# Kernel optimization log

Hardware: AMD Instinct MI355X
Metric: run time of the kernel (lower is better)

The kernel has to match this reference:

```python
import jax, jax.numpy as jnp
import numpy as np

# Dims: B samples, D=2048 backbone feature dim (resnet50 fc.in_features),
B, D, G, R, K, C = 16384, 2048, 8, 6, 3, 16


def setup_inputs() -> dict:
    key = jax.random.key(0)
    k0, k1, k2, k3 = jax.random.split(key, 4)
    feats = jax.random.normal(k0, (B, D), dtype=jnp.float32)          # backbone output (dropout=eval identity)
    roi_ids = jax.random.randint(k1, (B,), 0, G)                       # per-sample routing id (roi_names)
    W_reg = jax.random.normal(k2, (G, R, D), dtype=jnp.float32) * 0.02  # reg_heads[roi].weight
    b_reg = jnp.zeros((G, R), dtype=jnp.float32)                       # reg_heads[roi].bias
    W_cls = jax.random.normal(k3, (G, K, C, D), dtype=jnp.float32) * 0.02  # cls_heads[roi][k].weight
    b_cls = jnp.zeros((G, K, C), dtype=jnp.float32)                    # cls_heads[roi][k].bias
    return {"feats": feats, "roi_ids": roi_ids, "W_reg": W_reg, "b_reg": b_reg,
            "W_cls": W_cls, "b_cls": b_cls}


def reference(feats, roi_ids, W_reg, b_reg, W_cls, b_cls):
    # Original loop applies, per sample i, the Linear heads of roi_names[i].
    # Vectorized: compute all-ROI head outputs densely, then gather the routed one.
    # (Same math per sample; dropout is identity in eval mode.)
    reg_all = jnp.einsum('bd,grd->bgr', feats, W_reg) + b_reg[None]        # [B, G, R]
    cls_all = jnp.einsum('bd,gkcd->bgkc', feats, W_cls) + b_cls[None]      # [B, G, K, C]
    reg = jnp.take_along_axis(reg_all, roi_ids[:, None, None], axis=1)[:, 0]            # [B, R]
    cls = jnp.take_along_axis(cls_all, roi_ids[:, None, None, None], axis=1)[:, 0]      # [B, K, C]
    return reg, cls
```

## Files before the change

kernel.cpp:

```cpp
#include <hip/hip_runtime.h>
#include <hip/hip_bf16.h>

#define NB   16384
#define NG   8
#define ND   2048
#define NR   6
#define NKC  48
#define NOUT 54
#define NT16 (NB / 16 + NG)
#define LROW 136
#define BM   32
#define KC   128
#define NCH  (ND / KC)
#define MAXT (NB / BM + NG)

typedef __attribute__((ext_vector_type(8))) short short8_t;
typedef __attribute__((ext_vector_type(4))) float f32x4;

__device__ __forceinline__ unsigned short f2bf(float x) {
    union { float f; unsigned u; } v; v.f = x;
    unsigned r = v.u + 0x7FFFu + ((v.u >> 16) & 1u);
    return (unsigned short)(r >> 16);
}

__device__ __forceinline__ short8_t cvt8(float4 a, float4 b) {
    short8_t s;
    s[0] = (short)f2bf(a.x); s[1] = (short)f2bf(a.y);
    s[2] = (short)f2bf(a.z); s[3] = (short)f2bf(a.w);
    s[4] = (short)f2bf(b.x); s[5] = (short)f2bf(b.y);
    s[6] = (short)f2bf(b.z); s[7] = (short)f2bf(b.w);
    return s;
}

__device__ __forceinline__ void gl_lds16(const void* g, void* s) {
    __builtin_amdgcn_global_load_lds(
        (const __attribute__((address_space(1))) void*)g,
        (__attribute__((address_space(3))) void*)s,
        16, 0, 0);
}

#define WAITV(N) do { asm volatile("s_waitcnt vmcnt(" #N ")" ::: "memory"); \
                      __builtin_amdgcn_sched_barrier(0); } while (0)
#define BAR() do { __builtin_amdgcn_s_barrier(); \
                   __builtin_amdgcn_sched_barrier(0); } while (0)

__global__ void hist_kernel(const int* __restrict__ roi, int* __restrict__ counts) {
    int i = blockIdx.x * 256 + threadIdx.x;
    int g = roi[i];
    int lane = threadIdx.x & 63;
    #pragma unroll
    for (int gg = 0; gg < NG; ++gg) {
        unsigned long long m = __ballot(g == gg);
        if (m && lane == (int)(__ffsll((unsigned long long)m) - 1))
            atomicAdd(&counts[gg], (int)__popcll(m));
    }
}

__global__ void scatter_kernel(const int* __restrict__ roi, const int* __restrict__ counts,
                               int* __restrict__ ranks, int* __restrict__ perm) {
    int off[NG];
    int acc = 0;
    #pragma unroll
    for (int gg = 0; gg < NG; ++gg) { off[gg] = acc; acc += counts[gg]; }
    int i = blockIdx.x * 256 + threadIdx.x;
    int g = roi[i];
    int lane = threadIdx.x & 63;
    #pragma unroll
    for (int gg = 0; gg < NG; ++gg) {
        unsigned long long m = __ballot(g == gg);
        if (!m) continue;
        int leader = (int)(__ffsll((unsigned long long)m) - 1);
        int base = 0;
        if (lane == leader) base = atomicAdd(&ranks[gg], (int)__popcll(m));
        base = __shfl(base, leader);
        if (g == gg) {
            int rank = (int)__popcll(m & ((1ull << lane) - 1ull));
            perm[off[gg] + base + rank] = i;
        }
    }
}

__global__ void prep_kernel(const int* __restrict__ roi, int* __restrict__ cnt,
                            int* __restrict__ perm,
                            const float* __restrict__ Wreg, const float* __restrict__ Wcls,
                            short* __restrict__ Wbf) {
    if (blockIdx.x < 64) {
        int i = blockIdx.x * 256 + threadIdx.x;
        int g = roi[i];
        int lane = threadIdx.x & 63;
        #pragma unroll
        for (int gg = 0; gg < NG; ++gg) {
            unsigned long long m = __ballot(g == gg);
            if (!m) continue;
            int leader = (int)(__ffsll((unsigned long long)m) - 1);
            int base = 0;
            if (lane == leader) base = atomicAdd(&cnt[gg], (int)__popcll(m));
            base = __shfl(base, leader);
            if (g == gg) {
                int rank = (int)__popcll(m & ((1ull << lane) - 1ull));
                perm[gg * NB + base + rank] = i;
            }
        }
    } else {
        int u = (blockIdx.x - 64) * 256 + threadIdx.x;
        int l = u & 63;
        int q = (u >> 6) & 7;
        int c = (u >> 9) & 31;
        int g = u >> 14;
        int n = q >> 1, ks = q & 1;
        int row = n * 16 + (l & 15);
        int k   = c * 64 + ks * 32 + (l >> 4) * 8;
        short8_t v = {0, 0, 0, 0, 0, 0, 0, 0};
        if (row < NOUT) {
            const float* s = (row < NR) ? Wreg + (size_t)(g * NR + row) * ND + k
                                        : Wcls + (size_t)(g * NKC + row - NR) * ND + k;
            float4 a = *(const float4*)s;
            float4 b = *(const float4*)(s + 4);
            v = cvt8(a, b);
        }
        *(short8_t*)(Wbf + (size_t)u * 8) = v;
    }
}

__launch_bounds__(256, 4)
__global__ void gemm16_kernel(const float* __restrict__ feats,
                              const short* __restrict__ Wbf,
                              const float* __restrict__ breg, const float* __restrict__ bcls,
                              const int* __restrict__ cnt, const int* __restrict__ perm,
                              float* __restrict__ out) {
    __shared__ __align__(16) char lds[3][12288];
    __shared__ int sRow[16];

    int tid = threadIdx.x, w = tid >> 6, l = tid & 63, lr = l & 15, lq = l >> 4;

    int ts[NG + 1]; ts[0] = 0;
    #pragma unroll
    for (int gg = 0; gg < NG; ++gg) ts[gg + 1] = ts[gg] + ((cnt[gg] + 15) >> 4);
    int b = blockIdx.x;
    if (b >= ts[NG]) return;
    int g = 0;
    #pragma unroll
    for (int gg = 0; gg < NG; ++gg) if (b >= ts[gg + 1]) g = gg + 1;
    int cg = cnt[g];
    int rbase = (b - ts[g]) * 16;
    int nv = cg - rbase; if (nv > 16) nv = 16;

    if (tid < 16) {
        int r = rbase + tid;
        if (r >= cg) r = cg - 1;
        sRow[tid] = perm[g * NB + r];
    }
    __syncthreads();

    int srow = 4 * w + lq;
    const char* aSrc = (const char*)(feats + (size_t)sRow[srow] * ND)
                     + (((l & 15) ^ (srow & 7)) << 4);
    const char* bSrc = (const char*)Wbf + (size_t)g * 262144 + (2 * w) * 1024 + l * 16;

    const int key = lr & 7;
    const int ra00 = lr * 256 + (((0 * 8 + lq * 2 + 0) ^ key) << 4);
    const int ra01 = lr * 256 + (((0 * 8 + lq * 2 + 1) ^ key) << 4);
    const int ra10 = lr * 256 + (((1 * 8 + lq * 2 + 0) ^ key) << 4);
    const int ra11 = lr * 256 + (((1 * 8 + lq * 2 + 1) ^ key) << 4);
    const int rb0  = 4096 + (2 * w + 0) * 1024 + l * 16;
    const int rb1  = 4096 + (2 * w + 1) * 1024 + l * 16;

#define STAGE(cc, sl) do {                                                     \
        gl_lds16(aSrc + (size_t)(cc) * 256, &lds[sl][w * 1024]);               \
        const char* b_ = bSrc + (size_t)(cc) * 8192;                           \
        gl_lds16(b_,        &lds[sl][4096 + 2 * w * 1024]);                    \
        gl_lds16(b_ + 1024, &lds[sl][4096 + 2 * w * 1024 + 1024]);             \
    } while (0)

    f32x4 acc = {0, 0, 0, 0};

    STAGE(0, 0); STAGE(1, 1);
    int csl = 0;
    #pragma unroll
    for (int c = 0; c < 32; ++c) {
        if (c + 2 < 32) STAGE(c + 2, (c + 2) % 3);
        if (c < 30)       WAITV(6);
        else if (c == 30) WAITV(3);
        else              WAITV(0);
        BAR();
        {
            const char* s = &lds[csl][0];
            float4 a0 = *(const float4*)(s + ra00);
            float4 a1 = *(const float4*)(s + ra01);
            short8_t af0 = cvt8(a0, a1);
            short8_t b0  = *(const short8_t*)(s + rb0);
            acc = __builtin_amdgcn_mfma_f32_16x16x32_bf16(af0, b0, acc, 0, 0, 0);
            float4 a2 = *(const float4*)(s + ra10);
            float4 a3 = *(const float4*)(s + ra11);
            short8_t af1 = cvt8(a2, a3);
            short8_t b1  = *(const short8_t*)(s + rb1);
            acc = __builtin_amdgcn_mfma_f32_16x16x32_bf16(af1, b1, acc, 0, 0, 0);
        }
        BAR();
        csl = (csl == 2) ? 0 : csl + 1;
    }
#undef STAGE

    const int B6 = NB * NR;
    int col = w * 16 + lr;
    if (col < NOUT) {
        #pragma unroll
        for (int j = 0; j < 4; ++j) {
            int row = lq * 4 + j;
            if (row < nv) {
                int smp = sRow[row];
                if (col < NR) out[smp * NR + col] = acc[j] + breg[g * NR + col];
                else          out[B6 + smp * NKC + (col - NR)] = acc[j] + bcls[g * NKC + (col - NR)];
            }
        }
    }
}

__launch_bounds__(256, 3)
__global__ void gemm_kernel(const float* __restrict__ feats,
                            const float* __restrict__ Wreg, const float* __restrict__ breg,
                            const float* __restrict__ Wcls, const float* __restrict__ bcls,
                            const int* __restrict__ counts, const int* __restrict__ perm,
                            float* __restrict__ out, int stride) {
    __shared__ __align__(16) short Bsh[2][64][LROW];
    __shared__ int sRow[BM];

    int ts[NG + 1]; ts[0] = 0;
    int off[NG]; int acc = 0;
    #pragma unroll
    for (int gg = 0; gg < NG; ++gg) {
        int c = counts[gg];
        off[gg] = stride ? gg * stride : acc;
        acc += c;
        ts[gg + 1] = ts[gg] + (c + BM - 1) / BM;
    }
    int b = blockIdx.x;
    if (b >= ts[NG]) return;
    int g = 0;
    #pragma unroll
    for (int gg = 0; gg < NG; ++gg) if (b >= ts[gg + 1]) g = gg + 1;
    int gcnt  = counts[g];
    int goff  = off[g];
    int rbase = (b - ts[g]) * BM;
    int nvalid = gcnt - rbase; if (nvalid > BM) nvalid = BM;

    int tid = threadIdx.x;
    if (tid < BM) {
        int r = rbase + tid;
        if (r >= gcnt) r = gcnt - 1;
        sRow[tid] = perm[goff + r];
    }
    __syncthreads();

    int rB = tid >> 2;
    int cq = tid & 3;
    const float* wsrc = nullptr;
    if (rB < NR)        wsrc = Wreg + ((size_t)g * NR + rB) * ND + cq * 32;
    else if (rB < NOUT) wsrc = Wcls + ((size_t)g * NKC + (rB - NR)) * ND + cq * 32;

    int w = tid >> 6, l = tid & 63, lr = l & 15, lq = l >> 4;
    int mt = w & 1, nh = w >> 1;
    const float* aptr = feats + (size_t)sRow[mt * 16 + lr] * ND + lq * 8;
    const short* brp = (const short*)&Bsh[0][0][0] + (nh * 32 + lr) * LROW + lq * 8;

    f32x4 acc0 = {0, 0, 0, 0}, acc1 = {0, 0, 0, 0};
    float4 rb[8];

    if (wsrc) {
        #pragma unroll
        for (int i = 0; i < 8; ++i) rb[i] = *(const float4*)(wsrc + 4 * i);
    } else {
        #pragma unroll
        for (int i = 0; i < 8; ++i) rb[i] = make_float4(0.f, 0.f, 0.f, 0.f);
    }
    {
        short* bw = &Bsh[0][rB][cq * 32];
        #pragma unroll
        for (int j = 0; j < 4; ++j) *(short8_t*)(bw + 8 * j) = cvt8(rb[2 * j], rb[2 * j + 1]);
    }
    __syncthreads();

    #pragma unroll
    for (int c = 0; c < NCH; ++c) {
        const int cur = c & 1, nxt = cur ^ 1;
        if (c + 1 < NCH && wsrc) {
            const float* s = wsrc + (c + 1) * KC;
            #pragma unroll
            for (int i = 0; i < 8; ++i) rb[i] = *(const float4*)(s + 4 * i);
        }
        const short* bp = brp + cur * (64 * LROW);
        const float* ap = aptr + c * KC;
        #pragma unroll
        for (int ks = 0; ks < 4; ++ks) {
            float4 a0 = *(const float4*)(ap + ks * 32);
            float4 a1 = *(const float4*)(ap + ks * 32 + 4);
            short8_t af = cvt8(a0, a1);
            short8_t b0 = *(const short8_t*)(bp + ks * 32);
            short8_t b1 = *(const short8_t*)(bp + 16 * LROW + ks * 32);
            acc0 = __builtin_amdgcn_mfma_f32_16x16x32_bf16(af, b0, acc0, 0, 0, 0);
            acc1 = __builtin_amdgcn_mfma_f32_16x16x32_bf16(af, b1, acc1, 0, 0, 0);
        }
        if (c + 1 < NCH && wsrc) {
            short* bw = &Bsh[nxt][rB][cq * 32];
            #pragma unroll
            for (int j = 0; j < 4; ++j) *(short8_t*)(bw + 8 * j) = cvt8(rb[2 * j], rb[2 * j + 1]);
        } else if (c + 1 < NCH) {
            short8_t z = {0,0,0,0,0,0,0,0};
            short* bw = &Bsh[nxt][rB][cq * 32];
            #pragma unroll
            for (int j = 0; j < 4; ++j) *(short8_t*)(bw + 8 * j) = z;
        }
        __syncthreads();
    }

    const int B6 = NB * NR;
    #pragma unroll
    for (int n = 0; n < 2; ++n) {
        f32x4 v = n ? acc1 : acc0;
        int col = nh * 32 + n * 16 + lr;
        if (col < NOUT) {
            #pragma unroll
            for (int j = 0; j < 4; ++j) {
                int row = mt * 16 + lq * 4 + j;
                if (row < nvalid) {
                    int smp = sRow[row];
                    if (col < NR) out[smp * NR + col] = v[j] + breg[g * NR + col];
                    else          out[B6 + smp * NKC + (col - NR)] = v[j] + bcls[g * NKC + (col - NR)];
                }
            }
        }
    }
}

__global__ void fallback_kernel(const float* __restrict__ feats, const int* __restrict__ roi,
                                const float* __restrict__ Wreg, const float* __restrict__ breg,
                                const float* __restrict__ Wcls, const float* __restrict__ bcls,
                                float* __restrict__ out) {
    int i = blockIdx.x;
    int lane = threadIdx.x;
    int g = roi[i];
    const float* frow = feats + (size_t)i * ND;
    float f[32];
    #pragma unroll
    for (int q = 0; q < 32; ++q) f[q] = frow[lane + 64 * q];
    for (int o = 0; o < NOUT; ++o) {
        const float* wrow = (o < NR) ? Wreg + ((size_t)g * NR + o) * ND
                                     : Wcls + ((size_t)g * NKC + (o - NR)) * ND;
        float p = 0.f;
        #pragma unroll
        for (int q = 0; q < 32; ++q) p += f[q] * wrow[lane + 64 * q];
        #pragma unroll
        for (int s = 32; s; s >>= 1) p += __shfl_xor(p, s);
        if (lane == 0) {
            if (o < NR) out[i * NR + o] = p + breg[g * NR + o];
            else        out[NB * NR + i * NKC + (o - NR)] = p + bcls[g * NKC + (o - NR)];
        }
    }
}

extern "C" void kernel_launch(void* const* d_in, const int* in_sizes, int n_in,
                              void* d_out, int out_size, void* d_ws, size_t ws_size,
                              hipStream_t stream) {
    const float* feats = (const float*)d_in[0];
    const int*   roi   = (const int*)d_in[1];
    const float* Wreg  = (const float*)d_in[2];
    const float* breg  = (const float*)d_in[3];
    const float* Wcls  = (const float*)d_in[4];
    const float* bcls  = (const float*)d_in[5];
    float* out = (float*)d_out;

    const size_t wbfBytes = (size_t)NG * 131072 * 2;
    const size_t need_t1 = wbfBytes + 256 + (size_t)NG * NB * 4;
    const size_t need_t3 = 256 + (size_t)NB * 4;

    if (ws_size >= need_t1) {
        short* Wbf = (short*)d_ws;
        int* cnt   = (int*)((char*)d_ws + wbfBytes);
        int* perm  = cnt + 64;
        hipMemsetAsync(cnt, 0, 64, stream);
        prep_kernel<<<576, 256, 0, stream>>>(roi, cnt, perm, Wreg, Wcls, Wbf);
        gemm16_kernel<<<NT16, 256, 0, stream>>>(feats, Wbf, breg, bcls, cnt, perm, out);
    } else if (ws_size >= need_t3) {
        int* counts = (int*)d_ws;
        int* ranks  = counts + 8;
        int* perm   = counts + 64;
        hipMemsetAsync(counts, 0, 16 * sizeof(int), stream);
        hist_kernel<<<NB / 256, 256, 0, stream>>>(roi, counts);
        scatter_kernel<<<NB / 256, 256, 0, stream>>>(roi, counts, ranks, perm);
        gemm_kernel<<<MAXT, 256, 0, stream>>>(feats, Wreg, breg, Wcls, bcls, counts, perm, out, 0);
    } else {
        fallback_kernel<<<NB, 64, 0, stream>>>(feats, roi, Wreg, breg, Wcls, bcls, out);
    }
}
```

Baseline: 73.81 us.

## Replace 16-row GEMM with 64-row split-K tiles and six-stage LDS pipeline

```diff
diff --git a/kernel.cpp b/kernel.cpp
--- a/kernel.cpp
+++ b/kernel.cpp
@@ -7,7 +7,6 @@
 #define NR   6
 #define NKC  48
 #define NOUT 54
-#define NT16 (NB / 16 + NG)
 #define LROW 136
 #define BM   32
 #define KC   128
@@ -122,95 +121,107 @@
     }
 }
 
-__launch_bounds__(256, 4)
-__global__ void gemm16_kernel(const float* __restrict__ feats,
-                              const short* __restrict__ Wbf,
-                              const float* __restrict__ breg, const float* __restrict__ bcls,
-                              const int* __restrict__ cnt, const int* __restrict__ perm,
-                              float* __restrict__ out) {
-    __shared__ __align__(16) char lds[3][12288];
-    __shared__ int sRow[16];
+__launch_bounds__(512, 1)
+__global__ void gemm_d6_kernel(const float* __restrict__ feats,
+                               const short* __restrict__ Wbf,
+                               const float* __restrict__ breg, const float* __restrict__ bcls,
+                               const int* __restrict__ cnt, const int* __restrict__ perm,
+                               float* __restrict__ out) {
+    __shared__ __align__(16) char lds[6][24576];
+    __shared__ int sRow[64];
 
     int tid = threadIdx.x, w = tid >> 6, l = tid & 63, lr = l & 15, lq = l >> 4;
+    int rw = w >> 1, ch = w & 1;
 
     int ts[NG + 1]; ts[0] = 0;
     #pragma unroll
-    for (int gg = 0; gg < NG; ++gg) ts[gg + 1] = ts[gg] + ((cnt[gg] + 15) >> 4);
-    int b = blockIdx.x;
-    if (b >= ts[NG]) return;
+    for (int gg = 0; gg < NG; ++gg) ts[gg + 1] = ts[gg] + ((cnt[gg] + 63) >> 6);
+    int item = blockIdx.x;
+    if (item >= 2 * ts[NG]) return;
+    int t = item >> 1, kh = item & 1;
     int g = 0;
     #pragma unroll
-    for (int gg = 0; gg < NG; ++gg) if (b >= ts[gg + 1]) g = gg + 1;
+    for (int gg = 0; gg < NG; ++gg) if (t >= ts[gg + 1]) g = gg + 1;
     int cg = cnt[g];
-    int rbase = (b - ts[g]) * 16;
-    int nv = cg - rbase; if (nv > 16) nv = 16;
-
-    if (tid < 16) {
+    int rbase = (t - ts[g]) * 64;
+    int nv = cg - rbase; if (nv > 64) nv = 64;
+
+    if (tid < 64) {
         int r = rbase + tid;
         if (r >= cg) r = cg - 1;
         sRow[tid] = perm[g * NB + r];
     }
     __syncthreads();
 
-    int srow = 4 * w + lq;
-    const char* aSrc = (const char*)(feats + (size_t)sRow[srow] * ND)
-                     + (((l & 15) ^ (srow & 7)) << 4);
-    const char* bSrc = (const char*)Wbf + (size_t)g * 262144 + (2 * w) * 1024 + l * 16;
-
+    int r0 = 8 * w + (l >> 4), r1 = r0 + 4;
+    const char* a0c = (const char*)(feats + (size_t)sRow[r0] * ND) + kh * 4096
+                    + (((l & 15) ^ (r0 & 7)) << 4);
+    const char* a1c = (const char*)(feats + (size_t)sRow[r1] * ND) + kh * 4096
+                    + (((l & 15) ^ (r1 & 7)) << 4);
+    const char* bSrc = (const char*)Wbf + ((size_t)(g * 32 + kh * 16) * 8 + w) * 1024 + l * 16;
+
+#define STAGE(cc, sl) do {                                                     \
+        gl_lds16(a0c + (size_t)(cc) * 256,  &lds[sl][w * 2048]);               \
+        gl_lds16(a1c + (size_t)(cc) * 256,  &lds[sl][w * 2048 + 1024]);        \
+        gl_lds16(bSrc + (size_t)(cc) * 8192, &lds[sl][16384 + w * 1024]);      \
+    } while (0)
+
+    f32x4 acc0 = {0, 0, 0, 0}, acc1 = {0, 0, 0, 0};
+
+    STAGE(0, 0); STAGE(1, 1); STAGE(2, 2); STAGE(3, 3);
+
+    const int abase = (rw * 16 + lr) * 256;
     const int key = lr & 7;
-    const int ra00 = lr * 256 + (((0 * 8 + lq * 2 + 0) ^ key) << 4);
-    const int ra01 = lr * 256 + (((0 * 8 + lq * 2 + 1) ^ key) << 4);
-    const int ra10 = lr * 256 + (((1 * 8 + lq * 2 + 0) ^ key) << 4);
-    const int ra11 = lr * 256 + (((1 * 8 + lq * 2 + 1) ^ key) << 4);
-    const int rb0  = 4096 + (2 * w + 0) * 1024 + l * 16;
-    const int rb1  = 4096 + (2 * w + 1) * 1024 + l * 16;
-
-#define STAGE(cc, sl) do {                                                     \
-        gl_lds16(aSrc + (size_t)(cc) * 256, &lds[sl][w * 1024]);               \
-        const char* b_ = bSrc + (size_t)(cc) * 8192;                           \
-        gl_lds16(b_,        &lds[sl][4096 + 2 * w * 1024]);                    \
-        gl_lds16(b_ + 1024, &lds[sl][4096 + 2 * w * 1024 + 1024]);             \
-    } while (0)
-
-    f32x4 acc = {0, 0, 0, 0};
-
-    STAGE(0, 0); STAGE(1, 1);
-    int csl = 0;
-    #pragma unroll
-    for (int c = 0; c < 32; ++c) {
-        if (c + 2 < 32) STAGE(c + 2, (c + 2) % 3);
-        if (c < 30)       WAITV(6);
-        else if (c == 30) WAITV(3);
+    const int bq0 = 16384 + ((2 * ch + 0) * 2) * 1024 + l * 16;
+    const int bq1 = 16384 + ((2 * ch + 1) * 2) * 1024 + l * 16;
+
+    #pragma unroll
+    for (int c = 0; c < 16; ++c) {
+        const int sl = c % 6;
+        if (c < 12) STAGE(c + 4, (c + 4) % 6);
+        if (c < 12)       WAITV(12);
+        else if (c == 12) WAITV(9);
+        else if (c == 13) WAITV(6);
+        else if (c == 14) WAITV(3);
         else              WAITV(0);
         BAR();
         {
-            const char* s = &lds[csl][0];
-            float4 a0 = *(const float4*)(s + ra00);
-            float4 a1 = *(const float4*)(s + ra01);
+            const char* s = &lds[sl][0];
+            float4 a0 = *(const float4*)(s + abase + (((lq * 2 + 0) ^ key) << 4));
+            float4 a1 = *(const float4*)(s + abase + (((lq * 2 + 1) ^ key) << 4));
             short8_t af0 = cvt8(a0, a1);
-            short8_t b0  = *(const short8_t*)(s + rb0);
-            acc = __builtin_amdgcn_mfma_f32_16x16x32_bf16(af0, b0, acc, 0, 0, 0);
-            float4 a2 = *(const float4*)(s + ra10);
-            float4 a3 = *(const float4*)(s + ra11);
+            short8_t b00 = *(const short8_t*)(s + bq0);
+            short8_t b10 = *(const short8_t*)(s + bq1);
+            acc0 = __builtin_amdgcn_mfma_f32_16x16x32_bf16(af0, b00, acc0, 0, 0, 0);
+            acc1 = __builtin_amdgcn_mfma_f32_16x16x32_bf16(af0, b10, acc1, 0, 0, 0);
+            float4 a2 = *(const float4*)(s + abase + (((8 + lq * 2 + 0) ^ key) << 4));
+            float4 a3 = *(const float4*)(s + abase + (((8 + lq * 2 + 1) ^ key) << 4));
             short8_t af1 = cvt8(a2, a3);
-            short8_t b1  = *(const short8_t*)(s + rb1);
-            acc = __builtin_amdgcn_mfma_f32_16x16x32_bf16(af1, b1, acc, 0, 0, 0);
+            short8_t b01 = *(const short8_t*)(s + bq0 + 1024);
+            short8_t b11 = *(const short8_t*)(s + bq1 + 1024);
+            acc0 = __builtin_amdgcn_mfma_f32_16x16x32_bf16(af1, b01, acc0, 0, 0, 0);
+            acc1 = __builtin_amdgcn_mfma_f32_16x16x32_bf16(af1, b11, acc1, 0, 0, 0);
         }
         BAR();
-        csl = (csl == 2) ? 0 : csl + 1;
     }
 #undef STAGE
 
     const int B6 = NB * NR;
-    int col = w * 16 + lr;
-    if (col < NOUT) {
-        #pragma unroll
-        for (int j = 0; j < 4; ++j) {
-            int row = lq * 4 + j;
-            if (row < nv) {
-                int smp = sRow[row];
-                if (col < NR) out[smp * NR + col] = acc[j] + breg[g * NR + col];
-                else          out[B6 + smp * NKC + (col - NR)] = acc[j] + bcls[g * NKC + (col - NR)];
+    #pragma unroll
+    for (int cn = 0; cn < 2; ++cn) {
+        f32x4 v = cn ? acc1 : acc0;
+        int col = ch * 32 + cn * 16 + lr;
+        if (col < NOUT) {
+            float bias = 0.f;
+            if (kh == 0) bias = (col < NR) ? breg[g * NR + col] : bcls[g * NKC + (col - NR)];
+            #pragma unroll
+            for (int j = 0; j < 4; ++j) {
+                int row = rw * 16 + lq * 4 + j;
+                if (row < nv) {
+                    int smp = sRow[row];
+                    if (col < NR) atomicAdd(&out[smp * NR + col], v[j] + bias);
+                    else          atomicAdd(&out[B6 + smp * NKC + (col - NR)], v[j] + bias);
+                }
             }
         }
     }
@@ -377,9 +388,10 @@
         short* Wbf = (short*)d_ws;
         int* cnt   = (int*)((char*)d_ws + wbfBytes);
         int* perm  = cnt + 64;
+        hipMemsetAsync(out, 0, (size_t)out_size * sizeof(float), stream);
         hipMemsetAsync(cnt, 0, 64, stream);
         prep_kernel<<<576, 256, 0, stream>>>(roi, cnt, perm, Wreg, Wcls, Wbf);
-        gemm16_kernel<<<NT16, 256, 0, stream>>>(feats, Wbf, breg, bcls, cnt, perm, out);
+        gemm_d6_kernel<<<528, 512, 0, stream>>>(feats, Wbf, breg, bcls, cnt, perm, out);
     } else if (ws_size >= need_t3) {
         int* counts = (int*)d_ws;
         int* ranks  = counts + 8;
```

New measurement: 85.95 us. 1.16x slower.

## Load whole 16-row feature tile into LDS once, stream per-wave weights without barriers

Applied to the files above, without the earlier changes.

```diff
diff --git a/kernel.cpp b/kernel.cpp
--- a/kernel.cpp
+++ b/kernel.cpp
@@ -8,6 +8,8 @@
 #define NKC  48
 #define NOUT 54
 #define NT16 (NB / 16 + NG)
+#define AOFF 131072
+#define LDSZ (AOFF + 4 * 3 * 2048)
 #define LROW 136
 #define BM   32
 #define KC   128
@@ -103,12 +105,12 @@
         }
     } else {
         int u = (blockIdx.x - 64) * 256 + threadIdx.x;
-        int l = u & 63;
-        int q = (u >> 6) & 7;
-        int c = (u >> 9) & 31;
-        int g = u >> 14;
-        int n = q >> 1, ks = q & 1;
-        int row = n * 16 + (l & 15);
+        int l  = u & 63;
+        int ks = (u >> 6) & 1;
+        int c  = (u >> 7) & 31;
+        int w  = (u >> 12) & 3;
+        int g  = u >> 14;
+        int row = w * 16 + (l & 15);
         int k   = c * 64 + ks * 32 + (l >> 4) * 8;
         short8_t v = {0, 0, 0, 0, 0, 0, 0, 0};
         if (row < NOUT) {
@@ -122,13 +124,13 @@
     }
 }
 
-__launch_bounds__(256, 4)
-__global__ void gemm16_kernel(const float* __restrict__ feats,
-                              const short* __restrict__ Wbf,
-                              const float* __restrict__ breg, const float* __restrict__ bcls,
-                              const int* __restrict__ cnt, const int* __restrict__ perm,
-                              float* __restrict__ out) {
-    __shared__ __align__(16) char lds[3][12288];
+__launch_bounds__(256, 1)
+__global__ void gemm_res_kernel(const float* __restrict__ feats,
+                                const short* __restrict__ Wbf,
+                                const float* __restrict__ breg, const float* __restrict__ bcls,
+                                const int* __restrict__ cnt, const int* __restrict__ perm,
+                                float* __restrict__ out) {
+    __shared__ __align__(16) char lds[LDSZ];
     __shared__ int sRow[16];
 
     int tid = threadIdx.x, w = tid >> 6, l = tid & 63, lr = l & 15, lq = l >> 4;
@@ -142,6 +144,7 @@
     #pragma unroll
     for (int gg = 0; gg < NG; ++gg) if (b >= ts[gg + 1]) g = gg + 1;
     int cg = cnt[g];
+    if (cg <= 0) return;
     int rbase = (b - ts[g]) * 16;
     int nv = cg - rbase; if (nv > 16) nv = 16;
 
@@ -152,65 +155,63 @@
     }
     __syncthreads();
 
-    int srow = 4 * w + lq;
-    const char* aSrc = (const char*)(feats + (size_t)sRow[srow] * ND)
-                     + (((l & 15) ^ (srow & 7)) << 4);
-    const char* bSrc = (const char*)Wbf + (size_t)g * 262144 + (2 * w) * 1024 + l * 16;
-
+    const char* f = (const char*)feats;
+    const char* bSrc = (const char*)Wbf + (size_t)(g * 4 + w) * 32 * 2048 + l * 16;
+    char* Bb = lds + AOFF + w * 6144;
+
+    #pragma unroll
+    for (int rr = 0; rr < 4; ++rr) {
+        const int r = 4 * w + rr;
+        const char* src = f + (size_t)sRow[r] * 8192 + ((l ^ (r & 7)) << 4);
+        char* dst = lds + r * 8192;
+        #pragma unroll
+        for (int kk = 0; kk < 8; ++kk)
+            gl_lds16(src + kk * 1024, dst + kk * 1024);
+    }
+    gl_lds16(bSrc,        Bb);
+    gl_lds16(bSrc + 1024, Bb + 1024);
+    gl_lds16(bSrc + 2048, Bb + 2048);
+    gl_lds16(bSrc + 3072, Bb + 3072);
+    WAITV(2);
+    BAR();
+
+    f32x4 acc = {0, 0, 0, 0};
     const int key = lr & 7;
-    const int ra00 = lr * 256 + (((0 * 8 + lq * 2 + 0) ^ key) << 4);
-    const int ra01 = lr * 256 + (((0 * 8 + lq * 2 + 1) ^ key) << 4);
-    const int ra10 = lr * 256 + (((1 * 8 + lq * 2 + 0) ^ key) << 4);
-    const int ra11 = lr * 256 + (((1 * 8 + lq * 2 + 1) ^ key) << 4);
-    const int rb0  = 4096 + (2 * w + 0) * 1024 + l * 16;
-    const int rb1  = 4096 + (2 * w + 1) * 1024 + l * 16;
-
-#define STAGE(cc, sl) do {                                                     \
-        gl_lds16(aSrc + (size_t)(cc) * 256, &lds[sl][w * 1024]);               \
-        const char* b_ = bSrc + (size_t)(cc) * 8192;                           \
-        gl_lds16(b_,        &lds[sl][4096 + 2 * w * 1024]);                    \
-        gl_lds16(b_ + 1024, &lds[sl][4096 + 2 * w * 1024 + 1024]);             \
-    } while (0)
-
-    f32x4 acc = {0, 0, 0, 0};
-
-    STAGE(0, 0); STAGE(1, 1);
-    int csl = 0;
+    const char* Arow = lds + lr * 8192;
+
     #pragma unroll
     for (int c = 0; c < 32; ++c) {
-        if (c + 2 < 32) STAGE(c + 2, (c + 2) % 3);
-        if (c < 30)       WAITV(6);
-        else if (c == 30) WAITV(3);
-        else              WAITV(0);
-        BAR();
-        {
-            const char* s = &lds[csl][0];
-            float4 a0 = *(const float4*)(s + ra00);
-            float4 a1 = *(const float4*)(s + ra01);
-            short8_t af0 = cvt8(a0, a1);
-            short8_t b0  = *(const short8_t*)(s + rb0);
-            acc = __builtin_amdgcn_mfma_f32_16x16x32_bf16(af0, b0, acc, 0, 0, 0);
-            float4 a2 = *(const float4*)(s + ra10);
-            float4 a3 = *(const float4*)(s + ra11);
-            short8_t af1 = cvt8(a2, a3);
-            short8_t b1  = *(const short8_t*)(s + rb1);
-            acc = __builtin_amdgcn_mfma_f32_16x16x32_bf16(af1, b1, acc, 0, 0, 0);
-        }
-        BAR();
-        csl = (csl == 2) ? 0 : csl + 1;
-    }
-#undef STAGE
+        const int sl = c % 3;
+        if (c + 2 < 32) {
+            const char* bs = bSrc + (size_t)(c + 2) * 2048;
+            char* bd = Bb + ((c + 2) % 3) * 2048;
+            gl_lds16(bs, bd);
+            gl_lds16(bs + 1024, bd + 1024);
+            WAITV(4);
+        } else if (c == 30) { WAITV(2); }
+        else                { WAITV(0); }
+        #pragma unroll
+        for (int ks = 0; ks < 2; ++ks) {
+            const int U0 = c * 16 + ks * 8 + lq * 2;
+            float4 a0 = *(const float4*)(Arow + ((U0 ^ key) << 4));
+            float4 a1 = *(const float4*)(Arow + (((U0 + 1) ^ key) << 4));
+            short8_t af = cvt8(a0, a1);
+            short8_t bf = *(const short8_t*)(Bb + sl * 2048 + ks * 1024 + l * 16);
+            acc = __builtin_amdgcn_mfma_f32_16x16x32_bf16(af, bf, acc, 0, 0, 0);
+        }
+    }
 
     const int B6 = NB * NR;
     int col = w * 16 + lr;
     if (col < NOUT) {
+        float bias = (col < NR) ? breg[g * NR + col] : bcls[g * NKC + (col - NR)];
         #pragma unroll
         for (int j = 0; j < 4; ++j) {
             int row = lq * 4 + j;
             if (row < nv) {
                 int smp = sRow[row];
-                if (col < NR) out[smp * NR + col] = acc[j] + breg[g * NR + col];
-                else          out[B6 + smp * NKC + (col - NR)] = acc[j] + bcls[g * NKC + (col - NR)];
+                if (col < NR) out[smp * NR + col] = acc[j] + bias;
+                else          out[B6 + smp * NKC + (col - NR)] = acc[j] + bias;
             }
         }
     }
@@ -379,7 +380,7 @@
         int* perm  = cnt + 64;
         hipMemsetAsync(cnt, 0, 64, stream);
         prep_kernel<<<576, 256, 0, stream>>>(roi, cnt, perm, Wreg, Wcls, Wbf);
-        gemm16_kernel<<<NT16, 256, 0, stream>>>(feats, Wbf, breg, bcls, cnt, perm, out);
+        gemm_res_kernel<<<NT16, 256, 0, stream>>>(feats, Wbf, breg, bcls, cnt, perm, out);
     } else if (ws_size >= need_t3) {
         int* counts = (int*)d_ws;
         int* ranks  = counts + 8;
```

New measurement: 119.2 us. +61.5%, slower.

## Pre-cast and gather features into bf16 contiguous buffer, use 32-row GEMM tiles

Applied to the files above, without the earlier changes.

```diff
diff --git a/kernel.cpp b/kernel.cpp
--- a/kernel.cpp
+++ b/kernel.cpp
@@ -7,7 +7,7 @@
 #define NR   6
 #define NKC  48
 #define NOUT 54
-#define NT16 (NB / 16 + NG)
+#define NT32 (NB / 32 + NG)
 #define LROW 136
 #define BM   32
 #define KC   128
@@ -81,7 +81,7 @@
 }
 
 __global__ void prep_kernel(const int* __restrict__ roi, int* __restrict__ cnt,
-                            int* __restrict__ perm,
+                            int* __restrict__ rank,
                             const float* __restrict__ Wreg, const float* __restrict__ Wcls,
                             short* __restrict__ Wbf) {
     if (blockIdx.x < 64) {
@@ -97,8 +97,8 @@
             if (lane == leader) base = atomicAdd(&cnt[gg], (int)__popcll(m));
             base = __shfl(base, leader);
             if (g == gg) {
-                int rank = (int)__popcll(m & ((1ull << lane) - 1ull));
-                perm[gg * NB + base + rank] = i;
+                int r = (int)__popcll(m & ((1ull << lane) - 1ull));
+                rank[i] = base + r;
             }
         }
     } else {
@@ -122,57 +122,72 @@
     }
 }
 
+__global__ void castgather_kernel(const float* __restrict__ feats,
+                                  const int* __restrict__ roi,
+                                  const int* __restrict__ cnt, const int* __restrict__ rank,
+                                  short* __restrict__ gathered, int* __restrict__ permp) {
+    int b = blockIdx.x;
+    int tid = threadIdx.x;
+    int g = roi[b];
+    int pre = 0;
+    #pragma unroll
+    for (int gg = 0; gg < NG; ++gg) if (gg < g) pre += cnt[gg];
+    int pos = pre + rank[b];
+    if (tid == 0) permp[pos] = b;
+    const float* src = feats + (size_t)b * ND + tid * 8;
+    float4 a0 = *(const float4*)(src);
+    float4 a1 = *(const float4*)(src + 4);
+    *(short8_t*)(gathered + (size_t)pos * ND + tid * 8) = cvt8(a0, a1);
+}
+
 __launch_bounds__(256, 4)
-__global__ void gemm16_kernel(const float* __restrict__ feats,
+__global__ void gemm_s_kernel(const short* __restrict__ gathered,
                               const short* __restrict__ Wbf,
                               const float* __restrict__ breg, const float* __restrict__ bcls,
-                              const int* __restrict__ cnt, const int* __restrict__ perm,
+                              const int* __restrict__ cnt, const int* __restrict__ permp,
                               float* __restrict__ out) {
     __shared__ __align__(16) char lds[3][12288];
-    __shared__ int sRow[16];
 
     int tid = threadIdx.x, w = tid >> 6, l = tid & 63, lr = l & 15, lq = l >> 4;
+    int mt = w >> 1, nh = w & 1;
 
     int ts[NG + 1]; ts[0] = 0;
-    #pragma unroll
-    for (int gg = 0; gg < NG; ++gg) ts[gg + 1] = ts[gg] + ((cnt[gg] + 15) >> 4);
+    int pre[NG]; int acc_ = 0;
+    #pragma unroll
+    for (int gg = 0; gg < NG; ++gg) {
+        pre[gg] = acc_;
+        acc_ += cnt[gg];
+        ts[gg + 1] = ts[gg] + ((cnt[gg] + 31) >> 5);
+    }
     int b = blockIdx.x;
     if (b >= ts[NG]) return;
     int g = 0;
     #pragma unroll
     for (int gg = 0; gg < NG; ++gg) if (b >= ts[gg + 1]) g = gg + 1;
-    int cg = cnt[g];
-    int rbase = (b - ts[g]) * 16;
-    int nv = cg - rbase; if (nv > 16) nv = 16;
-
-    if (tid < 16) {
-        int r = rbase + tid;
-        if (r >= cg) r = cg - 1;
-        sRow[tid] = perm[g * NB + r];
-    }
-    __syncthreads();
-
-    int srow = 4 * w + lq;
-    const char* aSrc = (const char*)(feats + (size_t)sRow[srow] * ND)
-                     + (((l & 15) ^ (srow & 7)) << 4);
-    const char* bSrc = (const char*)Wbf + (size_t)g * 262144 + (2 * w) * 1024 + l * 16;
-
-    const int key = lr & 7;
-    const int ra00 = lr * 256 + (((0 * 8 + lq * 2 + 0) ^ key) << 4);
-    const int ra01 = lr * 256 + (((0 * 8 + lq * 2 + 1) ^ key) << 4);
-    const int ra10 = lr * 256 + (((1 * 8 + lq * 2 + 0) ^ key) << 4);
-    const int ra11 = lr * 256 + (((1 * 8 + lq * 2 + 1) ^ key) << 4);
-    const int rb0  = 4096 + (2 * w + 0) * 1024 + l * 16;
-    const int rb1  = 4096 + (2 * w + 1) * 1024 + l * 16;
+    int rbase = (b - ts[g]) * 32;
+    int nv = cnt[g] - rbase; if (nv > 32) nv = 32;
+    int t32 = pre[g] + rbase;
+
+    int rr = w * 8 + (l >> 3);
+    const char* aSrc = (const char*)gathered + ((size_t)t32 + rr) * 4096
+                     + (((l & 7) ^ (rr & 7)) << 4);
+    const char* bSrc = (const char*)Wbf + (size_t)g * 262144 + 2 * w * 1024 + l * 16;
+
+    const int ra0 = (mt * 16 + lr) * 128 + ((((0 * 4) + lq) ^ (lr & 7)) << 4);
+    const int ra1 = (mt * 16 + lr) * 128 + ((((1 * 4) + lq) ^ (lr & 7)) << 4);
+    const int rb00 = 4096 + ((nh * 2 + 0) * 2 + 0) * 1024 + l * 16;
+    const int rb01 = 4096 + ((nh * 2 + 0) * 2 + 1) * 1024 + l * 16;
+    const int rb10 = 4096 + ((nh * 2 + 1) * 2 + 0) * 1024 + l * 16;
+    const int rb11 = 4096 + ((nh * 2 + 1) * 2 + 1) * 1024 + l * 16;
 
 #define STAGE(cc, sl) do {                                                     \
-        gl_lds16(aSrc + (size_t)(cc) * 256, &lds[sl][w * 1024]);               \
+        gl_lds16(aSrc + (size_t)(cc) * 128, &lds[sl][w * 1024 + l * 16]);      \
         const char* b_ = bSrc + (size_t)(cc) * 8192;                           \
-        gl_lds16(b_,        &lds[sl][4096 + 2 * w * 1024]);                    \
-        gl_lds16(b_ + 1024, &lds[sl][4096 + 2 * w * 1024 + 1024]);             \
+        gl_lds16(b_,        &lds[sl][4096 + 2 * w * 1024 + l * 16]);           \
+        gl_lds16(b_ + 1024, &lds[sl][4096 + 2 * w * 1024 + 1024 + l * 16]);    \
     } while (0)
 
-    f32x4 acc = {0, 0, 0, 0};
+    f32x4 acc0 = {0, 0, 0, 0}, acc1 = {0, 0, 0, 0};
 
     STAGE(0, 0); STAGE(1, 1);
     int csl = 0;
@@ -185,16 +200,16 @@
         BAR();
         {
             const char* s = &lds[csl][0];
-            float4 a0 = *(const float4*)(s + ra00);
-            float4 a1 = *(const float4*)(s + ra01);
-            short8_t af0 = cvt8(a0, a1);
-            short8_t b0  = *(const short8_t*)(s + rb0);
-            acc = __builtin_amdgcn_mfma_f32_16x16x32_bf16(af0, b0, acc, 0, 0, 0);
-            float4 a2 = *(const float4*)(s + ra10);
-            float4 a3 = *(const float4*)(s + ra11);
-            short8_t af1 = cvt8(a2, a3);
-            short8_t b1  = *(const short8_t*)(s + rb1);
-            acc = __builtin_amdgcn_mfma_f32_16x16x32_bf16(af1, b1, acc, 0, 0, 0);
+            short8_t af0 = *(const short8_t*)(s + ra0);
+            short8_t b00 = *(const short8_t*)(s + rb00);
+            short8_t b10 = *(const short8_t*)(s + rb10);
+            acc0 = __builtin_amdgcn_mfma_f32_16x16x32_bf16(af0, b00, acc0, 0, 0, 0);
+            acc1 = __builtin_amdgcn_mfma_f32_16x16x32_bf16(af0, b10, acc1, 0, 0, 0);
+            short8_t af1 = *(const short8_t*)(s + ra1);
+            short8_t b01 = *(const short8_t*)(s + rb01);
+            short8_t b11 = *(const short8_t*)(s + rb11);
+            acc0 = __builtin_amdgcn_mfma_f32_16x16x32_bf16(af1, b01, acc0, 0, 0, 0);
+            acc1 = __builtin_amdgcn_mfma_f32_16x16x32_bf16(af1, b11, acc1, 0, 0, 0);
         }
         BAR();
         csl = (csl == 2) ? 0 : csl + 1;
@@ -202,15 +217,20 @@
 #undef STAGE
 
     const int B6 = NB * NR;
-    int col = w * 16 + lr;
-    if (col < NOUT) {
-        #pragma unroll
-        for (int j = 0; j < 4; ++j) {
-            int row = lq * 4 + j;
-            if (row < nv) {
-                int smp = sRow[row];
-                if (col < NR) out[smp * NR + col] = acc[j] + breg[g * NR + col];
-                else          out[B6 + smp * NKC + (col - NR)] = acc[j] + bcls[g * NKC + (col - NR)];
+    #pragma unroll
+    for (int cn = 0; cn < 2; ++cn) {
+        f32x4 v = cn ? acc1 : acc0;
+        int col = nh * 32 + cn * 16 + lr;
+        if (col < NOUT) {
+            float bias = (col < NR) ? breg[g * NR + col] : bcls[g * NKC + (col - NR)];
+            #pragma unroll
+            for (int j = 0; j < 4; ++j) {
+                int row = mt * 16 + lq * 4 + j;
+                if (row < nv) {
+                    int smp = permp[t32 + row];
+                    if (col < NR) out[smp * NR + col] = v[j] + bias;
+                    else          out[B6 + smp * NKC + (col - NR)] = v[j] + bias;
+                }
             }
         }
     }
@@ -370,16 +390,23 @@
     float* out = (float*)d_out;
 
     const size_t wbfBytes = (size_t)NG * 131072 * 2;
-    const size_t need_t1 = wbfBytes + 256 + (size_t)NG * NB * 4;
-    const size_t need_t3 = 256 + (size_t)NB * 4;
+    const size_t cntOff   = 2u * 1024 * 1024;
+    const size_t rankOff  = cntOff + 256;
+    const size_t permOff  = rankOff + (size_t)NB * 4;
+    const size_t gathOff  = 4u * 1024 * 1024;
+    const size_t need_t1  = gathOff + (size_t)(NB + 32) * 4096;
+    const size_t need_t3  = 256 + (size_t)NB * 4;
 
     if (ws_size >= need_t1) {
-        short* Wbf = (short*)d_ws;
-        int* cnt   = (int*)((char*)d_ws + wbfBytes);
-        int* perm  = cnt + 64;
+        short* Wbf     = (short*)d_ws;
+        int*   cnt     = (int*)((char*)d_ws + cntOff);
+        int*   rank    = (int*)((char*)d_ws + rankOff);
+        int*   permp   = (int*)((char*)d_ws + permOff);
+        short* gathered= (short*)((char*)d_ws + gathOff);
         hipMemsetAsync(cnt, 0, 64, stream);
-        prep_kernel<<<576, 256, 0, stream>>>(roi, cnt, perm, Wreg, Wcls, Wbf);
-        gemm16_kernel<<<NT16, 256, 0, stream>>>(feats, Wbf, breg, bcls, cnt, perm, out);
+        prep_kernel<<<576, 256, 0, stream>>>(roi, cnt, rank, Wreg, Wcls, Wbf);
+        castgather_kernel<<<NB, 256, 0, stream>>>(feats, roi, cnt, rank, gathered, permp);
+        gemm_s_kernel<<<NT32, 256, 0, stream>>>(gathered, Wbf, breg, bcls, cnt, permp, out);
     } else if (ws_size >= need_t3) {
         int* counts = (int*)d_ws;
         int* ranks  = counts + 8;
```

Measured after the change: 84.53 us. 14.5% more time.
